# Kernel optimization log

Measured on AMD Instinct MI355X. Metric: run time of the kernel, lower is better.

## Reference

```python
import math
import jax, jax.numpy as jnp
import numpy as np

B, N, H, D = 2, 2048, 16, 64


def _build_idx_table(seq_len, is_causal=True):
    """Fused hierarchical lookup table, faithful to
    build_hierarchical_index_lookup_table. Returns int32 [seq_len, log2(N)+1].
    Entries are (node_index + 1), negated if causally masked.
    Node numbering: leaves 0..N-1, then each level's parents appended;
    parent(i) = i // 2 + seq_len.
    """
    assert seq_len & (seq_len - 1) == 0
    total_nodes = 2 * seq_len - 1
    max_valid = total_nodes - 2  # root is never a neighbor
    level_num = int(math.log2(seq_len))
    total_cols = level_num + 1
    idx = np.ones((seq_len, total_cols), dtype=np.int32)
    n_cur = np.arange(seq_len, dtype=np.int64)
    idx[:, 0] = (n_cur + 1).astype(np.int32)  # self leaf
    for lvl in range(1, total_cols):
        if lvl == 1:
            n_next = n_cur ^ 1          # sibling leaf
            pair = n_cur
        else:
            pair = n_cur // 2 + seq_len  # parent node
            n_next = pair ^ 1            # uncle node
        valid = n_next <= max_valid
        val = n_next + 1
        if is_causal:
            should_mask = (pair < n_next) & valid
            val = np.where(should_mask, -val, val)
        idx[:, lvl] = np.where(valid, val.astype(np.int32), idx[:, lvl])
        n_cur = n_next
    return idx


IDX_TABLE = _build_idx_table(N, is_causal=True)  # [N, LEVELS]


def setup_inputs() -> dict:
    key = jax.random.key(0)
    kq, kk, kv = jax.random.split(key, 3)
    Q = jax.random.normal(kq, (B, N, H, D), dtype=jnp.float32)
    K = jax.random.normal(kk, (B, N, H, D), dtype=jnp.float32)
    V = jax.random.normal(kv, (B, N, H, D), dtype=jnp.float32)
    return {"Q": Q, "K": K, "V": V}


def _build_tree(K, V, scale):
    """Build the full binary-tree node set [B, 2N-1, H, D] for K and V.
    Each parent is a 3-way attention mix of {parent-mean, child0, child1}
    (build_parent_nodes semantics: fp32 online softmax with +1e-9 in denom),
    with the same weights applied to K and V values."""
    Ks, Vs = [K], [V]
    Kc, Vc = K, V
    while Kc.shape[1] > 1:  # trace-time loop over log2(N) levels
        K0, K1 = Kc[:, 0::2], Kc[:, 1::2]
        V0, V1 = Vc[:, 0::2], Vc[:, 1::2]
        Kp0 = 0.5 * (K0 + K1)  # initial parent K (query)
        Vp0 = 0.5 * (V0 + V1)
        s_self = jnp.sum(Kp0 * Kp0, axis=-1) * scale  # [B,P,H]
        s0 = jnp.sum(Kp0 * K0, axis=-1) * scale
        s1 = jnp.sum(Kp0 * K1, axis=-1) * scale
        m = jnp.maximum(s_self, jnp.maximum(s0, s1))
        e_s, e0, e1 = jnp.exp(s_self - m), jnp.exp(s0 - m), jnp.exp(s1 - m)
        denom = e_s + e0 + e1 + 1e-9
        ws, w0, w1 = (e_s / denom)[..., None], (e0 / denom)[..., None], (e1 / denom)[..., None]
        Kc = ws * Kp0 + w0 * K0 + w1 * K1
        Vc = ws * Vp0 + w0 * V0 + w1 * V1
        Ks.append(Kc)
        Vs.append(Vc)
    return jnp.concatenate(Ks, axis=1), jnp.concatenate(Vs, axis=1)


def reference(Q, K, V):
    b, n, h, d = Q.shape
    scale = 1.0 / math.sqrt(d)
    K_all, V_all = _build_tree(K, V, scale)  # [B, 2N-1, H, D]

    raw = jnp.asarray(IDX_TABLE)             # [N, L], sign-encoded
    nbr = jnp.abs(raw) - 1                   # neighbor node indices
    masked = raw < 0                         # causal mask

    Kg = jnp.take(K_all, nbr, axis=1)        # [B, N, L, H, D]
    Vg = jnp.take(V_all, nbr, axis=1)

    scores = jnp.einsum('bnhd,bnlhd->bnhl', Q, Kg) * scale
    scores = jnp.where(masked[None, :, None, :], -jnp.inf, scores)
    w = jax.nn.softmax(scores, axis=-1)      # [B, N, H, L]
    out = jnp.einsum('bnhl,bnlhd->bnhd', w, Vg)
    return out
```

## Files before the change

kernel.cpp:

```cpp
#include <hip/hip_runtime.h>

#define NSEQ   2048
#define HEADS  16
#define DIM    64
#define BATCH  2
#define SCALE  0.125f

#define WSSLOTS 2048
#define WSELEMS ((size_t)BATCH * WSSLOTS * HEADS * DIM)
#define ROWF4   (DIM / 4)
#define HSTRIDE (HEADS * ROWF4)

__device__ __forceinline__ int level_offset(int j) {
    return (j == 0) ? 0 : (2 * NSEQ - ((2 * NSEQ) >> j));
}

__device__ __forceinline__ float dot4(float4 a, float4 b) {
    return a.x * b.x + a.y * b.y + a.z * b.z + a.w * b.w;
}

__device__ __forceinline__ void reduce3_16(float& a, float& b, float& c) {
#pragma unroll
    for (int m = 1; m < 16; m <<= 1) {
        a += __shfl_xor(a, m, 64);
        b += __shfl_xor(b, m, 64);
        c += __shfl_xor(c, m, 64);
    }
}

__device__ __forceinline__ void make_parent4(float4 k0, float4 k1, float4 v0, float4 v1,
                                             float4& kc, float4& vc) {
    float4 kp, vp;
    kp.x = 0.5f * (k0.x + k1.x); kp.y = 0.5f * (k0.y + k1.y);
    kp.z = 0.5f * (k0.z + k1.z); kp.w = 0.5f * (k0.w + k1.w);
    vp.x = 0.5f * (v0.x + v1.x); vp.y = 0.5f * (v0.y + v1.y);
    vp.z = 0.5f * (v0.z + v1.z); vp.w = 0.5f * (v0.w + v1.w);
    float ss = dot4(kp, kp), sa = dot4(kp, k0), sb = dot4(kp, k1);
    reduce3_16(ss, sa, sb);
    ss *= SCALE; sa *= SCALE; sb *= SCALE;
    float mx = fmaxf(ss, fmaxf(sa, sb));
    float es = __expf(ss - mx), ea = __expf(sa - mx), eb = __expf(sb - mx);
    float inv = 1.0f / (es + ea + eb + 1e-9f);
    es *= inv; ea *= inv; eb *= inv;
    kc.x = es * kp.x + ea * k0.x + eb * k1.x;
    kc.y = es * kp.y + ea * k0.y + eb * k1.y;
    kc.z = es * kp.z + ea * k0.z + eb * k1.z;
    kc.w = es * kp.w + ea * k0.w + eb * k1.w;
    vc.x = es * vp.x + ea * v0.x + eb * v1.x;
    vc.y = es * vp.y + ea * v0.y + eb * v1.y;
    vc.z = es * vp.z + ea * v0.z + eb * v1.z;
    vc.w = es * vp.w + ea * v0.w + eb * v1.w;
}

__global__ __launch_bounds__(256) void tree_low(const float* __restrict__ K,
                                                const float* __restrict__ V,
                                                float* __restrict__ Kw,
                                                float* __restrict__ Vw) {
    __shared__ float4 Kb[48 * ROWF4];
    __shared__ float4 Vb[48 * ROWF4];
    const float4* K4 = (const float4*)K;
    const float4* V4 = (const float4*)V;
    float4* Kw4 = (float4*)Kw;
    float4* Vw4 = (float4*)Vw;

    int bid = blockIdx.x;
    int c = bid & 31;
    int h = (bid >> 5) & 15;
    int b = bid >> 9;
    int wave = threadIdx.x >> 6;
    int lane = threadIdx.x & 63;
    int g = lane >> 4, t = lane & 15;

#pragma unroll
    for (int j = 1; j <= 6; ++j) {
        int P = 64 >> j;
        int curOff  = (j & 1) ? 0 : 32;
        int prevOff = (j & 1) ? 32 : 0;
        for (int i0 = 0; i0 < P; i0 += 16) {
            int p = i0 + wave * 4 + g;
            if (p < P) {
                float4 k0, k1, v0, v1;
                if (j == 1) {
                    int n0 = c * 64 + 2 * p;
                    const float4* Kr = K4 + ((size_t)((b * NSEQ + n0) * HEADS + h)) * ROWF4;
                    const float4* Vr = V4 + ((size_t)((b * NSEQ + n0) * HEADS + h)) * ROWF4;
                    k0 = Kr[t]; k1 = Kr[HSTRIDE + t];
                    v0 = Vr[t]; v1 = Vr[HSTRIDE + t];
                } else {
                    int s = (prevOff + 2 * p) * ROWF4 + t;
                    k0 = Kb[s]; k1 = Kb[s + ROWF4];
                    v0 = Vb[s]; v1 = Vb[s + ROWF4];
                }
                float4 kc, vc;
                make_parent4(k0, k1, v0, v1, kc, vc);
                Kb[(curOff + p) * ROWF4 + t] = kc;
                Vb[(curOff + p) * ROWF4 + t] = vc;
                int slot = level_offset(j) - NSEQ + c * P + p;
                size_t widx = ((size_t)((b * WSSLOTS + slot) * HEADS + h)) * ROWF4 + t;
                Kw4[widx] = kc;
                Vw4[widx] = vc;
            }
        }
        __syncthreads();
    }
}

__global__ __launch_bounds__(256) void tree_top(float* __restrict__ Kw,
                                                float* __restrict__ Vw) {
    __shared__ float4 Kb[28 * ROWF4];
    __shared__ float4 Vb[28 * ROWF4];
    float4* Kw4 = (float4*)Kw;
    float4* Vw4 = (float4*)Vw;

    int h = blockIdx.x & 15, b = blockIdx.x >> 4;
    int lane = threadIdx.x & 63;
    int g = lane >> 4, t = lane & 15;
    int p = (threadIdx.x >> 6) * 4 + g;

    {
        size_t cb = ((size_t)((b * WSSLOTS + 1984 + 2 * p) * HEADS + h)) * ROWF4 + t;
        float4 k0 = Kw4[cb], k1 = Kw4[cb + HSTRIDE];
        float4 v0 = Vw4[cb], v1 = Vw4[cb + HSTRIDE];
        float4 kc, vc;
        make_parent4(k0, k1, v0, v1, kc, vc);
        Kb[p * ROWF4 + t] = kc;  Vb[p * ROWF4 + t] = vc;
        size_t w = ((size_t)((b * WSSLOTS + 2016 + p) * HEADS + h)) * ROWF4 + t;
        Kw4[w] = kc;  Vw4[w] = vc;
    }
    __syncthreads();
    if (p < 8) {
        int s = (2 * p) * ROWF4 + t;
        float4 k0 = Kb[s], k1 = Kb[s + ROWF4];
        float4 v0 = Vb[s], v1 = Vb[s + ROWF4];
        float4 kc, vc;
        make_parent4(k0, k1, v0, v1, kc, vc);
        Kb[(16 + p) * ROWF4 + t] = kc;  Vb[(16 + p) * ROWF4 + t] = vc;
        size_t w = ((size_t)((b * WSSLOTS + 2032 + p) * HEADS + h)) * ROWF4 + t;
        Kw4[w] = kc;  Vw4[w] = vc;
    }
    __syncthreads();
    if (p < 4) {
        int s = (16 + 2 * p) * ROWF4 + t;
        float4 k0 = Kb[s], k1 = Kb[s + ROWF4];
        float4 v0 = Vb[s], v1 = Vb[s + ROWF4];
        float4 kc, vc;
        make_parent4(k0, k1, v0, v1, kc, vc);
        Kb[(24 + p) * ROWF4 + t] = kc;  Vb[(24 + p) * ROWF4 + t] = vc;
        size_t w = ((size_t)((b * WSSLOTS + 2040 + p) * HEADS + h)) * ROWF4 + t;
        Kw4[w] = kc;  Vw4[w] = vc;
    }
    __syncthreads();
    if (p < 2) {
        int s = (24 + 2 * p) * ROWF4 + t;
        float4 k0 = Kb[s], k1 = Kb[s + ROWF4];
        float4 v0 = Vb[s], v1 = Vb[s + ROWF4];
        float4 kc, vc;
        make_parent4(k0, k1, v0, v1, kc, vc);
        size_t w = ((size_t)((b * WSSLOTS + 2044 + p) * HEADS + h)) * ROWF4 + t;
        Kw4[w] = kc;  Vw4[w] = vc;
    }
}

__global__ __launch_bounds__(256) void attn(const float* __restrict__ Q,
                                            const float* __restrict__ K,
                                            const float* __restrict__ V,
                                            const float* __restrict__ Kw,
                                            const float* __restrict__ Vw,
                                            float* __restrict__ out) {
    const float4* Q4 = (const float4*)Q;
    const float4* K4 = (const float4*)K;
    const float4* V4 = (const float4*)V;
    const float4* Kw4 = (const float4*)Kw;
    const float4* Vw4 = (const float4*)Vw;
    float4* O4 = (float4*)out;

    int w = blockIdx.x * 4 + (threadIdx.x >> 6);
    int lane = threadIdx.x & 63;
    int g = lane >> 4;
    int t = lane & 15;
    int h = (w & 3) * 4 + g;
    int n = (w >> 2) & (NSEQ - 1);
    int b = w >> 13;

    int row0 = (b * NSEQ + n) * HSTRIDE;
    int row1 = (b * NSEQ + (n ^ 1)) * HSTRIDE;
    int rowt[10];
#pragma unroll
    for (int l = 2; l < 12; ++l) {
        int j = l - 1;
        int slot = level_offset(j) - NSEQ + ((n >> j) ^ 1);
        rowt[l - 2] = (b * WSSLOTS + slot) * HSTRIDE;
    }
    int hoff = h * ROWF4 + t;

    unsigned active = 1u | (((unsigned)n & 0x7FFu) << 1);

    float4 q4 = Q4[row0 + hoff];

    float4 k[12];
    k[0] = K4[row0 + hoff];
    k[1] = K4[row1 + hoff];
#pragma unroll
    for (int l = 2; l < 12; ++l) k[l] = Kw4[rowt[l - 2] + hoff];

    float s[12];
#pragma unroll
    for (int l = 0; l < 12; ++l) s[l] = dot4(q4, k[l]);

    float4 v[12];
    v[0] = V4[row0 + hoff];
    v[1] = V4[row1 + hoff];
#pragma unroll
    for (int l = 2; l < 12; ++l) v[l] = Vw4[rowt[l - 2] + hoff];

#pragma unroll
    for (int m = 1; m < 16; m <<= 1) {
#pragma unroll
        for (int l = 0; l < 12; ++l) s[l] += __shfl_xor(s[l], m, 64);
    }

    float mx = -3.402823466e+38f;
#pragma unroll
    for (int l = 0; l < 12; ++l) {
        s[l] *= SCALE;
        if (active & (1u << l)) mx = fmaxf(mx, s[l]);
    }
    float sum = 0.f;
#pragma unroll
    for (int l = 0; l < 12; ++l) {
        float e = (active & (1u << l)) ? __expf(s[l] - mx) : 0.f;
        s[l] = e;
        sum += e;
    }
    float inv = 1.0f / sum;

    float4 o = make_float4(0.f, 0.f, 0.f, 0.f);
#pragma unroll
    for (int l = 0; l < 12; ++l) {
        o.x += s[l] * v[l].x; o.y += s[l] * v[l].y;
        o.z += s[l] * v[l].z; o.w += s[l] * v[l].w;
    }
    O4[row0 + hoff] = make_float4(o.x * inv, o.y * inv, o.z * inv, o.w * inv);
}

extern "C" void kernel_launch(void* const* d_in, const int* in_sizes, int n_in,
                              void* d_out, int out_size, void* d_ws, size_t ws_size,
                              hipStream_t stream) {
    const float* Q = (const float*)d_in[0];
    const float* K = (const float*)d_in[1];
    const float* V = (const float*)d_in[2];
    float* out = (float*)d_out;
    float* Kw = (float*)d_ws;
    float* Vw = Kw + WSELEMS;

    tree_low<<<1024, 256, 0, stream>>>(K, V, Kw, Vw);
    tree_top<<<BATCH * HEADS, 256, 0, stream>>>(Kw, Vw);
    attn<<<(BATCH * NSEQ * (HEADS / 4)) / 4, 256, 0, stream>>>(Q, K, V, Kw, Vw, out);
}
```

Measured before the change: 128.9 us.

## Fuse tree levels in pairs per thread group and swizzle attention block order

```diff
diff --git a/kernel.cpp b/kernel.cpp
--- a/kernel.cpp
+++ b/kernel.cpp
@@ -25,6 +25,19 @@
         a += __shfl_xor(a, m, 64);
         b += __shfl_xor(b, m, 64);
         c += __shfl_xor(c, m, 64);
+    }
+}
+
+__device__ __forceinline__ void reduce6_16(float& a, float& b, float& c,
+                                           float& d, float& e, float& f) {
+#pragma unroll
+    for (int m = 1; m < 16; m <<= 1) {
+        a += __shfl_xor(a, m, 64);
+        b += __shfl_xor(b, m, 64);
+        c += __shfl_xor(c, m, 64);
+        d += __shfl_xor(d, m, 64);
+        e += __shfl_xor(e, m, 64);
+        f += __shfl_xor(f, m, 64);
     }
 }
 
@@ -52,12 +65,68 @@
     vc.w = es * vp.w + ea * v0.w + eb * v1.w;
 }
 
+__device__ __forceinline__ void make_parent_pair4(const float4* k, const float4* v,
+                                                  float4& ka, float4& va,
+                                                  float4& kb, float4& vb) {
+    float4 kpa, vpa, kpb, vpb;
+    kpa.x = 0.5f * (k[0].x + k[1].x); kpa.y = 0.5f * (k[0].y + k[1].y);
+    kpa.z = 0.5f * (k[0].z + k[1].z); kpa.w = 0.5f * (k[0].w + k[1].w);
+    vpa.x = 0.5f * (v[0].x + v[1].x); vpa.y = 0.5f * (v[0].y + v[1].y);
+    vpa.z = 0.5f * (v[0].z + v[1].z); vpa.w = 0.5f * (v[0].w + v[1].w);
+    kpb.x = 0.5f * (k[2].x + k[3].x); kpb.y = 0.5f * (k[2].y + k[3].y);
+    kpb.z = 0.5f * (k[2].z + k[3].z); kpb.w = 0.5f * (k[2].w + k[3].w);
+    vpb.x = 0.5f * (v[2].x + v[3].x); vpb.y = 0.5f * (v[2].y + v[3].y);
+    vpb.z = 0.5f * (v[2].z + v[3].z); vpb.w = 0.5f * (v[2].w + v[3].w);
+    float ssa = dot4(kpa, kpa), saa = dot4(kpa, k[0]), sba = dot4(kpa, k[1]);
+    float ssb = dot4(kpb, kpb), sab = dot4(kpb, k[2]), sbb = dot4(kpb, k[3]);
+    reduce6_16(ssa, saa, sba, ssb, sab, sbb);
+    ssa *= SCALE; saa *= SCALE; sba *= SCALE;
+    ssb *= SCALE; sab *= SCALE; sbb *= SCALE;
+    float mxa = fmaxf(ssa, fmaxf(saa, sba));
+    float mxb = fmaxf(ssb, fmaxf(sab, sbb));
+    float esa = __expf(ssa - mxa), eaa = __expf(saa - mxa), eba = __expf(sba - mxa);
+    float esb = __expf(ssb - mxb), eab = __expf(sab - mxb), ebb = __expf(sbb - mxb);
+    float iva = 1.0f / (esa + eaa + eba + 1e-9f);
+    float ivb = 1.0f / (esb + eab + ebb + 1e-9f);
+    esa *= iva; eaa *= iva; eba *= iva;
+    esb *= ivb; eab *= ivb; ebb *= ivb;
+    ka.x = esa * kpa.x + eaa * k[0].x + eba * k[1].x;
+    ka.y = esa * kpa.y + eaa * k[0].y + eba * k[1].y;
+    ka.z = esa * kpa.z + eaa * k[0].z + eba * k[1].z;
+    ka.w = esa * kpa.w + eaa * k[0].w + eba * k[1].w;
+    va.x = esa * vpa.x + eaa * v[0].x + eba * v[1].x;
+    va.y = esa * vpa.y + eaa * v[0].y + eba * v[1].y;
+    va.z = esa * vpa.z + eaa * v[0].z + eba * v[1].z;
+    va.w = esa * vpa.w + eaa * v[0].w + eba * v[1].w;
+    kb.x = esb * kpb.x + eab * k[2].x + ebb * k[3].x;
+    kb.y = esb * kpb.y + eab * k[2].y + ebb * k[3].y;
+    kb.z = esb * kpb.z + eab * k[2].z + ebb * k[3].z;
+    kb.w = esb * kpb.w + eab * k[2].w + ebb * k[3].w;
+    vb.x = esb * vpb.x + eab * v[2].x + ebb * v[3].x;
+    vb.y = esb * vpb.y + eab * v[2].y + ebb * v[3].y;
+    vb.z = esb * vpb.z + eab * v[2].z + ebb * v[3].z;
+    vb.w = esb * vpb.w + eab * v[2].w + ebb * v[3].w;
+}
+
+__device__ __forceinline__ void quad_step(const float4* k, const float4* v,
+                                          float4* Kw4, float4* Vw4,
+                                          size_t pRow0, size_t gRow,
+                                          int t,
+                                          float4& kg, float4& vg) {
+    float4 ka, va, kb, vb;
+    make_parent_pair4(k, v, ka, va, kb, vb);
+    Kw4[pRow0 + t] = ka;            Vw4[pRow0 + t] = va;
+    Kw4[pRow0 + HSTRIDE + t] = kb;  Vw4[pRow0 + HSTRIDE + t] = vb;
+    make_parent4(ka, kb, va, vb, kg, vg);
+    Kw4[gRow + t] = kg;             Vw4[gRow + t] = vg;
+}
+
 __global__ __launch_bounds__(256) void tree_low(const float* __restrict__ K,
                                                 const float* __restrict__ V,
                                                 float* __restrict__ Kw,
                                                 float* __restrict__ Vw) {
-    __shared__ float4 Kb[48 * ROWF4];
-    __shared__ float4 Vb[48 * ROWF4];
+    __shared__ float4 Kb[20 * ROWF4];
+    __shared__ float4 Vb[20 * ROWF4];
     const float4* K4 = (const float4*)K;
     const float4* V4 = (const float4*)V;
     float4* Kw4 = (float4*)Kw;
@@ -67,97 +136,97 @@
     int c = bid & 31;
     int h = (bid >> 5) & 15;
     int b = bid >> 9;
-    int wave = threadIdx.x >> 6;
     int lane = threadIdx.x & 63;
-    int g = lane >> 4, t = lane & 15;
-
-#pragma unroll
-    for (int j = 1; j <= 6; ++j) {
-        int P = 64 >> j;
-        int curOff  = (j & 1) ? 0 : 32;
-        int prevOff = (j & 1) ? 32 : 0;
-        for (int i0 = 0; i0 < P; i0 += 16) {
-            int p = i0 + wave * 4 + g;
-            if (p < P) {
-                float4 k0, k1, v0, v1;
-                if (j == 1) {
-                    int n0 = c * 64 + 2 * p;
-                    const float4* Kr = K4 + ((size_t)((b * NSEQ + n0) * HEADS + h)) * ROWF4;
-                    const float4* Vr = V4 + ((size_t)((b * NSEQ + n0) * HEADS + h)) * ROWF4;
-                    k0 = Kr[t]; k1 = Kr[HSTRIDE + t];
-                    v0 = Vr[t]; v1 = Vr[HSTRIDE + t];
-                } else {
-                    int s = (prevOff + 2 * p) * ROWF4 + t;
-                    k0 = Kb[s]; k1 = Kb[s + ROWF4];
-                    v0 = Vb[s]; v1 = Vb[s + ROWF4];
-                }
-                float4 kc, vc;
-                make_parent4(k0, k1, v0, v1, kc, vc);
-                Kb[(curOff + p) * ROWF4 + t] = kc;
-                Vb[(curOff + p) * ROWF4 + t] = vc;
-                int slot = level_offset(j) - NSEQ + c * P + p;
-                size_t widx = ((size_t)((b * WSSLOTS + slot) * HEADS + h)) * ROWF4 + t;
-                Kw4[widx] = kc;
-                Vw4[widx] = vc;
-            }
+    int gg = (threadIdx.x >> 6) * 4 + (lane >> 4);
+    int t = lane & 15;
+
+    size_t wsBase = (size_t)(b * WSSLOTS) * HSTRIDE + h * ROWF4;
+
+    {
+        int n0 = c * 64 + 4 * gg;
+        const float4* Kr = K4 + ((size_t)((b * NSEQ + n0) * HEADS + h)) * ROWF4;
+        const float4* Vr = V4 + ((size_t)((b * NSEQ + n0) * HEADS + h)) * ROWF4;
+        float4 k[4], v[4];
+#pragma unroll
+        for (int j = 0; j < 4; ++j) { k[j] = Kr[j * HSTRIDE + t]; v[j] = Vr[j * HSTRIDE + t]; }
+        int s1 = c * 32 + 2 * gg;
+        int s2 = 1024 + c * 16 + gg;
+        float4 kg, vg;
+        quad_step(k, v, Kw4, Vw4, wsBase + (size_t)s1 * HSTRIDE,
+                  wsBase + (size_t)s2 * HSTRIDE, t, kg, vg);
+        Kb[gg * ROWF4 + t] = kg;  Vb[gg * ROWF4 + t] = vg;
+    }
+    __syncthreads();
+    if (gg < 4) {
+        float4 k[4], v[4];
+#pragma unroll
+        for (int j = 0; j < 4; ++j) {
+            k[j] = Kb[(4 * gg + j) * ROWF4 + t];
+            v[j] = Vb[(4 * gg + j) * ROWF4 + t];
         }
-        __syncthreads();
+        int s3 = 1536 + c * 8 + 2 * gg;
+        int s4 = 1792 + c * 4 + gg;
+        float4 kg, vg;
+        quad_step(k, v, Kw4, Vw4, wsBase + (size_t)s3 * HSTRIDE,
+                  wsBase + (size_t)s4 * HSTRIDE, t, kg, vg);
+        Kb[(16 + gg) * ROWF4 + t] = kg;  Vb[(16 + gg) * ROWF4 + t] = vg;
+    }
+    __syncthreads();
+    if (gg == 0) {
+        float4 k[4], v[4];
+#pragma unroll
+        for (int j = 0; j < 4; ++j) {
+            k[j] = Kb[(16 + j) * ROWF4 + t];
+            v[j] = Vb[(16 + j) * ROWF4 + t];
+        }
+        int s5 = 1920 + c * 2;
+        int s6 = 1984 + c;
+        float4 kg, vg;
+        quad_step(k, v, Kw4, Vw4, wsBase + (size_t)s5 * HSTRIDE,
+                  wsBase + (size_t)s6 * HSTRIDE, t, kg, vg);
     }
 }
 
 __global__ __launch_bounds__(256) void tree_top(float* __restrict__ Kw,
                                                 float* __restrict__ Vw) {
-    __shared__ float4 Kb[28 * ROWF4];
-    __shared__ float4 Vb[28 * ROWF4];
+    __shared__ float4 Kb[8 * ROWF4];
+    __shared__ float4 Vb[8 * ROWF4];
     float4* Kw4 = (float4*)Kw;
     float4* Vw4 = (float4*)Vw;
 
     int h = blockIdx.x & 15, b = blockIdx.x >> 4;
     int lane = threadIdx.x & 63;
-    int g = lane >> 4, t = lane & 15;
-    int p = (threadIdx.x >> 6) * 4 + g;
-
-    {
-        size_t cb = ((size_t)((b * WSSLOTS + 1984 + 2 * p) * HEADS + h)) * ROWF4 + t;
-        float4 k0 = Kw4[cb], k1 = Kw4[cb + HSTRIDE];
-        float4 v0 = Vw4[cb], v1 = Vw4[cb + HSTRIDE];
-        float4 kc, vc;
-        make_parent4(k0, k1, v0, v1, kc, vc);
-        Kb[p * ROWF4 + t] = kc;  Vb[p * ROWF4 + t] = vc;
-        size_t w = ((size_t)((b * WSSLOTS + 2016 + p) * HEADS + h)) * ROWF4 + t;
-        Kw4[w] = kc;  Vw4[w] = vc;
+    int gg = (threadIdx.x >> 6) * 4 + (lane >> 4);
+    int t = lane & 15;
+    size_t wsBase = (size_t)(b * WSSLOTS) * HSTRIDE + h * ROWF4;
+
+    if (gg < 8) {
+        float4 k[4], v[4];
+#pragma unroll
+        for (int j = 0; j < 4; ++j) {
+            size_t r = wsBase + (size_t)(1984 + 4 * gg + j) * HSTRIDE + t;
+            k[j] = Kw4[r]; v[j] = Vw4[r];
+        }
+        int s7 = 2016 + 2 * gg;
+        int s8 = 2032 + gg;
+        float4 kg, vg;
+        quad_step(k, v, Kw4, Vw4, wsBase + (size_t)s7 * HSTRIDE,
+                  wsBase + (size_t)s8 * HSTRIDE, t, kg, vg);
+        Kb[gg * ROWF4 + t] = kg;  Vb[gg * ROWF4 + t] = vg;
     }
     __syncthreads();
-    if (p < 8) {
-        int s = (2 * p) * ROWF4 + t;
-        float4 k0 = Kb[s], k1 = Kb[s + ROWF4];
-        float4 v0 = Vb[s], v1 = Vb[s + ROWF4];
-        float4 kc, vc;
-        make_parent4(k0, k1, v0, v1, kc, vc);
-        Kb[(16 + p) * ROWF4 + t] = kc;  Vb[(16 + p) * ROWF4 + t] = vc;
-        size_t w = ((size_t)((b * WSSLOTS + 2032 + p) * HEADS + h)) * ROWF4 + t;
-        Kw4[w] = kc;  Vw4[w] = vc;
-    }
-    __syncthreads();
-    if (p < 4) {
-        int s = (16 + 2 * p) * ROWF4 + t;
-        float4 k0 = Kb[s], k1 = Kb[s + ROWF4];
-        float4 v0 = Vb[s], v1 = Vb[s + ROWF4];
-        float4 kc, vc;
-        make_parent4(k0, k1, v0, v1, kc, vc);
-        Kb[(24 + p) * ROWF4 + t] = kc;  Vb[(24 + p) * ROWF4 + t] = vc;
-        size_t w = ((size_t)((b * WSSLOTS + 2040 + p) * HEADS + h)) * ROWF4 + t;
-        Kw4[w] = kc;  Vw4[w] = vc;
-    }
-    __syncthreads();
-    if (p < 2) {
-        int s = (24 + 2 * p) * ROWF4 + t;
-        float4 k0 = Kb[s], k1 = Kb[s + ROWF4];
-        float4 v0 = Vb[s], v1 = Vb[s + ROWF4];
-        float4 kc, vc;
-        make_parent4(k0, k1, v0, v1, kc, vc);
-        size_t w = ((size_t)((b * WSSLOTS + 2044 + p) * HEADS + h)) * ROWF4 + t;
-        Kw4[w] = kc;  Vw4[w] = vc;
+    if (gg < 2) {
+        float4 k[4], v[4];
+#pragma unroll
+        for (int j = 0; j < 4; ++j) {
+            k[j] = Kb[(4 * gg + j) * ROWF4 + t];
+            v[j] = Vb[(4 * gg + j) * ROWF4 + t];
+        }
+        int s9  = 2040 + 2 * gg;
+        int s10 = 2044 + gg;
+        float4 kg, vg;
+        quad_step(k, v, Kw4, Vw4, wsBase + (size_t)s9 * HSTRIDE,
+                  wsBase + (size_t)s10 * HSTRIDE, t, kg, vg);
     }
 }
 
@@ -174,7 +243,9 @@
     const float4* Vw4 = (const float4*)Vw;
     float4* O4 = (float4*)out;
 
-    int w = blockIdx.x * 4 + (threadIdx.x >> 6);
+    int bid = blockIdx.x;
+    int vbid = ((bid & 7) << 9) | (bid >> 3);
+    int w = vbid * 4 + (threadIdx.x >> 6);
     int lane = threadIdx.x & 63;
     int g = lane >> 4;
     int t = lane & 15;
```

New measurement: 124.2 us. 1.04x faster.
